# Kernel tuning notes

Measured on AMD Instinct MI355X. Metric: run time of the kernel, lower is better.

The kernel has to match this reference:

```python
import jax, jax.numpy as jnp
import numpy as np

N = 100000      # nodes
E = 1600000     # edges
F_IN = 64       # num_features
H = 64          # nhid
G = 512         # num graphs in batch
C = 2           # num_classes
BN_EPS = 1e-5


def setup_inputs() -> dict:
    key = jax.random.key(0)
    ks = jax.random.split(key, 8)
    x = jax.random.normal(ks[0], (N, F_IN), jnp.float32)
    edge_index = jax.random.randint(ks[1], (2, E), 0, N, dtype=jnp.int64)
    batch = jnp.sort(jax.random.randint(ks[2], (N,), 0, G, dtype=jnp.int64))
    s = lambda k, shp, fan: (jax.random.normal(k, shp, jnp.float32) / np.sqrt(fan)).astype(jnp.float32)
    W1 = s(ks[3], (F_IN, H), F_IN); b1 = jnp.zeros((H,), jnp.float32)
    W2 = s(ks[4], (H, H), H);       b2 = jnp.zeros((H,), jnp.float32)
    Wg = s(ks[5], (H, 1), H);       bg = jnp.zeros((1,), jnp.float32)
    bn_gamma = jnp.ones((H,), jnp.float32); bn_beta = jnp.zeros((H,), jnp.float32)
    bn_mean = jnp.zeros((H,), jnp.float32); bn_var = jnp.ones((H,), jnp.float32)
    W_lin = s(ks[6], (H, C), H);    b_lin = jnp.zeros((C,), jnp.float32)
    return dict(x=x, edge_index=edge_index, batch=batch,
                W1=W1, b1=b1, W2=W2, b2=b2, Wg=Wg, bg=bg,
                bn_gamma=bn_gamma, bn_beta=bn_beta, bn_mean=bn_mean, bn_var=bn_var,
                W_lin=W_lin, b_lin=b_lin)


def reference(x, edge_index, batch, W1, b1, W2, b2, Wg, bg,
              bn_gamma, bn_beta, bn_mean, bn_var, W_lin, b_lin):
    src, dst = edge_index[0], edge_index[1]
    # GINConv (eps=0): h_i = MLP(x_i + sum_{j->i} x_j)
    agg = jax.ops.segment_sum(x[src], dst, num_segments=N)       # [N, F_IN]
    h = x + agg
    h = jnp.maximum(h @ W1 + b1, 0.0) @ W2 + b2                  # [N, H]
    h = jnp.maximum(h, 0.0)                                      # outer ReLU
    # Attentional aggregation: segment softmax of gate, weighted segment-sum
    gate = (h @ Wg + bg)[:, 0]                                   # [N]
    gmax = jax.ops.segment_max(gate, batch, num_segments=G)      # [G]
    ex = jnp.exp(gate - gmax[batch])                             # [N]
    denom = jax.ops.segment_sum(ex, batch, num_segments=G)       # [G]
    alpha = ex / denom[batch]                                    # [N]
    pooled = jax.ops.segment_sum(alpha[:, None] * h, batch, num_segments=G)  # [G, H]
    # BatchNorm1d in eval mode (running stats); dropout is identity in eval
    norm = (pooled - bn_mean) / jnp.sqrt(bn_var + BN_EPS) * bn_gamma + bn_beta
    logits = norm @ W_lin + b_lin                                # [G, C]
    return jax.nn.log_softmax(logits, axis=-1)
```

## Files before the change

kernel.cpp:

```cpp
#include <hip/hip_runtime.h>
#include <math.h>
#include <float.h>

#define BN_EPS 1e-5f
#define PBLK   8192
#define NBUCKP 832
#define ACAP   4096
#define STCAP  2048

typedef short s16x8 __attribute__((ext_vector_type(8)));
typedef float f32x4 __attribute__((ext_vector_type(4)));

__device__ __forceinline__ unsigned short f2bf(float f) {
    unsigned u = __float_as_uint(f);
    u += 0x7FFFu + ((u >> 16) & 1u);
    return (unsigned short)(u >> 16);
}
__device__ __forceinline__ float bf2f(unsigned short b) {
    return __uint_as_float(((unsigned)b) << 16);
}

__global__ __launch_bounds__(512) void prep_partition(
    const float* __restrict__ x, unsigned short* __restrict__ xb,
    const float* __restrict__ W1, const float* __restrict__ W2,
    unsigned short* __restrict__ w1t, unsigned short* __restrict__ w2t,
    const int* __restrict__ src, const int* __restrict__ dst,
    const int* __restrict__ batch, int* __restrict__ gstart,
    int* __restrict__ bcur0, int* __restrict__ packed2,
    int N, int E, int EB, int G)
{
    __shared__ int hist[NBUCKP], lstart[NBUCKP], goff[NBUCKP], cur[NBUCKP];
    __shared__ int sorted[PBLK];
    __shared__ unsigned short sbkt[PBLK];

    int tid = threadIdx.x;
    int lane = tid & 63;
    int blk = blockIdx.x;

    int n4 = N * 16;
    for (int i = blk * 512 + tid; i < n4; i += gridDim.x * 512) {
        float4 f = *(const float4*)(x + (size_t)i * 4);
        ushort4 o;
        o.x = f2bf(f.x); o.y = f2bf(f.y); o.z = f2bf(f.z); o.w = f2bf(f.w);
        *(ushort4*)(xb + (size_t)i * 4) = o;
    }
    for (int i = blk * 512 + tid; i < N; i += gridDim.x * 512) {
        int bi = batch[i];
        int bp = (i == 0) ? -1 : batch[i - 1];
        for (int g = bp + 1; g <= bi; ++g) gstart[g] = i;
        if (i == N - 1)
            for (int g = bi + 1; g <= G; ++g) gstart[g] = N;
    }
    if (blk == 0)
        for (int idx = tid; idx < 4096; idx += 512)
            w1t[idx] = f2bf(W1[(idx & 63) * 64 + (idx >> 6)]);
    if (blk == 1)
        for (int idx = tid; idx < 4096; idx += 512)
            w2t[idx] = f2bf(W2[(idx & 63) * 64 + (idx >> 6)]);

    if (blk >= EB) return;

    int e0 = blk * PBLK;
    int cnt = E - e0; if (cnt > PBLK) cnt = PBLK; if (cnt < 0) cnt = 0;

    for (int i = tid; i < NBUCKP; i += 512) hist[i] = 0;
    __syncthreads();
    for (int i = tid; i < cnt; i += 512)
        atomicAdd(&hist[dst[e0 + i] >> 7], 1);
    __syncthreads();
    if (tid < 64) {
        int carry = 0;
        #pragma unroll
        for (int c = 0; c < NBUCKP / 64; ++c) {
            int idx = c * 64 + lane;
            int v = hist[idx];
            int xv = v;
            #pragma unroll
            for (int d = 1; d < 64; d <<= 1) {
                int t = __shfl_up(xv, d); if (lane >= d) xv += t;
            }
            lstart[idx] = xv - v + carry;
            carry += __shfl(xv, 63);
        }
    }
    __syncthreads();
    for (int i = tid; i < NBUCKP; i += 512) {
        cur[i] = lstart[i];
        if (hist[i] > 0) goff[i] = atomicAdd(&bcur0[i], hist[i]);
    }
    __syncthreads();
    for (int i = tid; i < cnt; i += 512) {
        int d = dst[e0 + i];
        int s = src[e0 + i];
        int b = d >> 7;
        int p = atomicAdd(&cur[b], 1);
        sorted[p] = ((d & 127) << 17) | s;
        sbkt[p] = (unsigned short)b;
    }
    __syncthreads();
    for (int i = tid; i < cnt; i += 512) {
        int b = sbkt[i];
        packed2[(size_t)b * ACAP + goff[b] + (i - lstart[b])] = sorted[i];
    }
}

__global__ __launch_bounds__(256) void bucket_fused(
    const unsigned short* __restrict__ xb,
    const int* __restrict__ packed2, const int* __restrict__ bcur0,
    const unsigned short* __restrict__ w1t, const unsigned short* __restrict__ w2t,
    const float* __restrict__ b1, const float* __restrict__ b2,
    const float* __restrict__ Wg, const float* __restrict__ bg,
    unsigned short* __restrict__ h_out, float* __restrict__ gate_out, int N)
{
    __shared__ int hist[64], excl[65], cur[64];
    __shared__ int stage[STCAP];
    __shared__ unsigned short vt[64][72];

    int tid = threadIdx.x;
    int lane = tid & 63;
    int wave = tid >> 6;
    int bh = blockIdx.x;
    int bk = bh >> 1;
    int half = bh & 1;
    int node0 = bh * 64;
    int ecnt = bcur0[bk];
    if (ecnt > ACAP) ecnt = ACAP;
    const int* arena = packed2 + (size_t)bk * ACAP;

    if (tid < 64) hist[tid] = 0;
    __syncthreads();
    for (int i = tid; i < ecnt; i += 256) {
        int v = arena[i];
        if ((v >> 23) == half)
            atomicAdd(&hist[(v >> 17) & 63], 1);
    }
    __syncthreads();
    if (tid < 64) {
        int v = hist[lane];
        int xv = v;
        #pragma unroll
        for (int d = 1; d < 64; d <<= 1) {
            int t = __shfl_up(xv, d); if (lane >= d) xv += t;
        }
        excl[lane] = xv - v;
        cur[lane]  = xv - v;
        if (lane == 63) excl[64] = xv;
    }
    __syncthreads();
    for (int i = tid; i < ecnt; i += 256) {
        int v = arena[i];
        if ((v >> 23) == half) {
            int p = atomicAdd(&cur[(v >> 17) & 63], 1);
            if (p < STCAP) stage[p] = v & 0x1FFFF;
        }
    }
    __syncthreads();

    int rowbase = wave * 16;
    for (int m = 0; m < 16; ++m) {
        int ln = rowbase + m;
        int node = node0 + ln;
        if (node < N) {
            int beg = excl[ln];     if (beg > STCAP) beg = STCAP;
            int end = excl[ln + 1]; if (end > STCAP) end = STCAP;

            float v0 = bf2f(xb[(size_t)node * 64 + lane]);
            float v1 = 0.f, v2 = 0.f, v3 = 0.f, v4 = 0.f, v5 = 0.f, v6 = 0.f, v7 = 0.f;

            for (int base = beg; base < end; base += 64) {
                int ei = (base + lane < end) ? stage[base + lane] : 0;
                int cnt = end - base; if (cnt > 64) cnt = 64;
                int j = 0;
                for (; j + 8 <= cnt; j += 8) {
                    int s0 = __builtin_amdgcn_readlane(ei, j + 0);
                    int s1 = __builtin_amdgcn_readlane(ei, j + 1);
                    int s2 = __builtin_amdgcn_readlane(ei, j + 2);
                    int s3 = __builtin_amdgcn_readlane(ei, j + 3);
                    int s4 = __builtin_amdgcn_readlane(ei, j + 4);
                    int s5 = __builtin_amdgcn_readlane(ei, j + 5);
                    int s6 = __builtin_amdgcn_readlane(ei, j + 6);
                    int s7 = __builtin_amdgcn_readlane(ei, j + 7);
                    unsigned short t0 = xb[(size_t)s0 * 64 + lane];
                    unsigned short t1 = xb[(size_t)s1 * 64 + lane];
                    unsigned short t2 = xb[(size_t)s2 * 64 + lane];
                    unsigned short t3 = xb[(size_t)s3 * 64 + lane];
                    unsigned short t4 = xb[(size_t)s4 * 64 + lane];
                    unsigned short t5 = xb[(size_t)s5 * 64 + lane];
                    unsigned short t6 = xb[(size_t)s6 * 64 + lane];
                    unsigned short t7 = xb[(size_t)s7 * 64 + lane];
                    v0 += bf2f(t0); v1 += bf2f(t1); v2 += bf2f(t2); v3 += bf2f(t3);
                    v4 += bf2f(t4); v5 += bf2f(t5); v6 += bf2f(t6); v7 += bf2f(t7);
                }
                for (; j + 4 <= cnt; j += 4) {
                    int s0 = __builtin_amdgcn_readlane(ei, j + 0);
                    int s1 = __builtin_amdgcn_readlane(ei, j + 1);
                    int s2 = __builtin_amdgcn_readlane(ei, j + 2);
                    int s3 = __builtin_amdgcn_readlane(ei, j + 3);
                    unsigned short t0 = xb[(size_t)s0 * 64 + lane];
                    unsigned short t1 = xb[(size_t)s1 * 64 + lane];
                    unsigned short t2 = xb[(size_t)s2 * 64 + lane];
                    unsigned short t3 = xb[(size_t)s3 * 64 + lane];
                    v4 += bf2f(t0); v5 += bf2f(t1); v6 += bf2f(t2); v7 += bf2f(t3);
                }
                for (; j < cnt; ++j) {
                    int s = __builtin_amdgcn_readlane(ei, j);
                    v1 += bf2f(xb[(size_t)s * 64 + lane]);
                }
            }
            float v = ((v0 + v1) + (v2 + v3)) + ((v4 + v5) + (v6 + v7));
            vt[ln][lane] = f2bf(v);
        } else {
            vt[ln][lane] = 0;
        }
    }

    {
        int quad = lane >> 4;
        int col  = lane & 15;

        s16x8 a0 = *(const s16x8*)&vt[rowbase + col][quad * 8];
        s16x8 a1 = *(const s16x8*)&vt[rowbase + col][32 + quad * 8];

        float b1v[4], b2v[4], wgv[4];
        #pragma unroll
        for (int nt = 0; nt < 4; ++nt) {
            b1v[nt] = b1[nt * 16 + col];
            b2v[nt] = b2[nt * 16 + col];
            wgv[nt] = Wg[nt * 16 + col];
        }
        float bgv = bg[0];

        f32x4 acc1[4];
        #pragma unroll
        for (int nt = 0; nt < 4; ++nt) {
            int off = (nt * 16 + col) * 64 + quad * 8;
            s16x8 w0 = *(const s16x8*)(w1t + off);
            s16x8 w1 = *(const s16x8*)(w1t + off + 32);
            f32x4 c = {0.f, 0.f, 0.f, 0.f};
            c = __builtin_amdgcn_mfma_f32_16x16x32_bf16(a0, w0, c, 0, 0, 0);
            c = __builtin_amdgcn_mfma_f32_16x16x32_bf16(a1, w1, c, 0, 0, 0);
            acc1[nt] = c;
        }
        #pragma unroll
        for (int nt = 0; nt < 4; ++nt)
            #pragma unroll
            for (int r = 0; r < 4; ++r) {
                float hv = fmaxf(acc1[nt][r] + b1v[nt], 0.f);
                vt[rowbase + quad * 4 + r][nt * 16 + col] = f2bf(hv);
            }

        s16x8 g0 = *(const s16x8*)&vt[rowbase + col][quad * 8];
        s16x8 g1 = *(const s16x8*)&vt[rowbase + col][32 + quad * 8];

        f32x4 acc2[4];
        #pragma unroll
        for (int nt = 0; nt < 4; ++nt) {
            int off = (nt * 16 + col) * 64 + quad * 8;
            s16x8 w0 = *(const s16x8*)(w2t + off);
            s16x8 w1 = *(const s16x8*)(w2t + off + 32);
            f32x4 c = {0.f, 0.f, 0.f, 0.f};
            c = __builtin_amdgcn_mfma_f32_16x16x32_bf16(g0, w0, c, 0, 0, 0);
            c = __builtin_amdgcn_mfma_f32_16x16x32_bf16(g1, w1, c, 0, 0, 0);
            acc2[nt] = c;
        }

        int nbase = node0 + rowbase;
        float gp[4] = {0.f, 0.f, 0.f, 0.f};
        #pragma unroll
        for (int nt = 0; nt < 4; ++nt)
            #pragma unroll
            for (int r = 0; r < 4; ++r) {
                float hv = fmaxf(acc2[nt][r] + b2v[nt], 0.f);
                int node = nbase + quad * 4 + r;
                if (node < N)
                    h_out[(size_t)node * 64 + nt * 16 + col] = f2bf(hv);
                gp[r] = fmaf(hv, wgv[nt], gp[r]);
            }
        #pragma unroll
        for (int r = 0; r < 4; ++r) {
            float t = gp[r];
            t += __shfl_xor(t, 1);
            t += __shfl_xor(t, 2);
            t += __shfl_xor(t, 4);
            t += __shfl_xor(t, 8);
            int node = nbase + quad * 4 + r;
            if (col == 0 && node < N) gate_out[node] = t + bgv;
        }
    }
}

__global__ __launch_bounds__(256) void pool_final(
    const unsigned short* __restrict__ h, const float* __restrict__ gate,
    const int* __restrict__ gstart,
    const float* __restrict__ gamma_, const float* __restrict__ beta_,
    const float* __restrict__ mean_, const float* __restrict__ var_,
    const float* __restrict__ Wl, const float* __restrict__ bl,
    float* __restrict__ out)
{
    int g = blockIdx.x;
    int tid = threadIdx.x;

    int start = gstart[g];
    int end   = gstart[g + 1];

    __shared__ float red[4];
    __shared__ float pool_s[4 * 64];

    int lane = tid & 63;
    int wave = tid >> 6;

    float m = -FLT_MAX;
    for (int i = start + tid; i < end; i += 256) m = fmaxf(m, gate[i]);
    #pragma unroll
    for (int off = 32; off; off >>= 1) m = fmaxf(m, __shfl_xor(m, off));
    if (lane == 0) red[wave] = m;
    __syncthreads();
    m = fmaxf(fmaxf(red[0], red[1]), fmaxf(red[2], red[3]));
    __syncthreads();

    float s = 0.f;
    for (int i = start + tid; i < end; i += 256) s += expf(gate[i] - m);
    #pragma unroll
    for (int off = 32; off; off >>= 1) s += __shfl_xor(s, off);
    if (lane == 0) red[wave] = s;
    __syncthreads();
    s = red[0] + red[1] + red[2] + red[3];

    float a0 = 0.f, a1 = 0.f, a2 = 0.f, a3 = 0.f;
    int i = start + wave;
    for (; i + 12 < end; i += 16) {
        float e0 = expf(gate[i]      - m);
        float e1 = expf(gate[i + 4]  - m);
        float e2 = expf(gate[i + 8]  - m);
        float e3 = expf(gate[i + 12] - m);
        float t0 = bf2f(h[(size_t)(i)      * 64 + lane]);
        float t1 = bf2f(h[(size_t)(i + 4)  * 64 + lane]);
        float t2 = bf2f(h[(size_t)(i + 8)  * 64 + lane]);
        float t3 = bf2f(h[(size_t)(i + 12) * 64 + lane]);
        a0 = fmaf(e0, t0, a0);
        a1 = fmaf(e1, t1, a1);
        a2 = fmaf(e2, t2, a2);
        a3 = fmaf(e3, t3, a3);
    }
    for (; i < end; i += 4) {
        float e = expf(gate[i] - m);
        a0 = fmaf(e, bf2f(h[(size_t)i * 64 + lane]), a0);
    }
    pool_s[wave * 64 + lane] = (a0 + a1) + (a2 + a3);
    __syncthreads();

    if (wave == 0) {
        float p = pool_s[lane] + pool_s[64 + lane] + pool_s[128 + lane] + pool_s[192 + lane];
        p = (end > start) ? (p / s) : 0.f;
        float nrm = (p - mean_[lane]) / sqrtf(var_[lane] + BN_EPS) * gamma_[lane] + beta_[lane];
        float l0 = nrm * Wl[lane * 2 + 0];
        float l1 = nrm * Wl[lane * 2 + 1];
        #pragma unroll
        for (int off = 32; off; off >>= 1) {
            l0 += __shfl_xor(l0, off);
            l1 += __shfl_xor(l1, off);
        }
        if (lane == 0) {
            l0 += bl[0];
            l1 += bl[1];
            float mx = fmaxf(l0, l1);
            float lse = mx + logf(expf(l0 - mx) + expf(l1 - mx));
            out[g * 2 + 0] = l0 - lse;
            out[g * 2 + 1] = l1 - lse;
        }
    }
}

extern "C" void kernel_launch(void* const* d_in, const int* in_sizes, int n_in,
                              void* d_out, int out_size, void* d_ws, size_t ws_size,
                              hipStream_t stream)
{
    const float* x     = (const float*)d_in[0];
    const int*   eidx  = (const int*)d_in[1];
    const int*   batch = (const int*)d_in[2];
    const float* W1    = (const float*)d_in[3];
    const float* b1    = (const float*)d_in[4];
    const float* W2    = (const float*)d_in[5];
    const float* b2    = (const float*)d_in[6];
    const float* Wg    = (const float*)d_in[7];
    const float* bg    = (const float*)d_in[8];
    const float* bng   = (const float*)d_in[9];
    const float* bnb   = (const float*)d_in[10];
    const float* bnm   = (const float*)d_in[11];
    const float* bnv   = (const float*)d_in[12];
    const float* Wl    = (const float*)d_in[13];
    const float* bl    = (const float*)d_in[14];
    float* out = (float*)d_out;

    int N = in_sizes[0] / 64;
    int E = in_sizes[1] / 2;
    int G = out_size / 2;
    int NP = ((N + 63) / 64) * 64;
    int NBUCK = (N + 127) / 128;
    int NHALF = (N + 63) / 64;
    int EB = (E + PBLK - 1) / PBLK;
    int GRID_A = 1024 > EB ? 1024 : EB;

    char* w = (char*)d_ws;
    int* packed2 = (int*)w;                     w += (size_t)NBUCK * ACAP * 4;
    unsigned short* hxb  = (unsigned short*)w;  w += (size_t)NP * 64 * 2;
    float* gate  = (float*)w;                   w += ((size_t)N * 4 + 255) / 256 * 256;
    int* bcur0   = (int*)w;                     w += NBUCKP * 4;
    unsigned short* w1t = (unsigned short*)w;   w += 4096 * 2;
    unsigned short* w2t = (unsigned short*)w;   w += 4096 * 2;
    int* gstart  = (int*)w;                     w += ((size_t)(G + 1) * 4 + 255) / 256 * 256;
    unsigned short* hbuf = (unsigned short*)w;

    const int* src = eidx;
    const int* dst = eidx + E;

    hipMemsetAsync(bcur0, 0, NBUCKP * sizeof(int), stream);

    prep_partition<<<GRID_A, 512, 0, stream>>>(x, hxb, W1, W2, w1t, w2t,
                                               src, dst, batch, gstart,
                                               bcur0, packed2,
                                               N, E, EB, G);

    bucket_fused  <<<NHALF, 256, 0, stream>>>(hxb, packed2, bcur0, w1t, w2t,
                                              b1, b2, Wg, bg, hbuf, gate, N);

    pool_final    <<<G, 256, 0, stream>>>(hbuf, gate, gstart, bng, bnb, bnm, bnv,
                                          Wl, bl, out);
}
```

Before: 216.0 us.

## Sort buckets in place per 128-node block and drop LDS staging

The partition kernel now uses smaller per-block chunks and scatters edges straight to the global bucket arenas, with no LDS sort-then-copy pass. The fused kernel now handles a whole 128-node bucket with 512 threads. It reads the arena once into registers, counting-sorts it back in place in global memory, and prefetches each node's next edge list while the current one is processed. The MFMA operand tile moves to an XOR-swizzled LDS layout to avoid bank conflicts. In exchange, the in-place global sort relies on the arena being private to each block, the scatter stores in the partition kernel are uncoalesced, and the 8-register edge capture assumes each bucket holds at most 4096 edges.

Measured after the change: 205.3 us. 1.05x faster.

```diff
diff --git a/kernel.cpp b/kernel.cpp
--- a/kernel.cpp
+++ b/kernel.cpp
@@ -3,10 +3,9 @@
 #include <float.h>
 
 #define BN_EPS 1e-5f
-#define PBLK   8192
+#define PBLK   2048
 #define NBUCKP 832
 #define ACAP   4096
-#define STCAP  2048
 
 typedef short s16x8 __attribute__((ext_vector_type(8)));
 typedef float f32x4 __attribute__((ext_vector_type(4)));
@@ -18,6 +17,9 @@
 }
 __device__ __forceinline__ float bf2f(unsigned short b) {
     return __uint_as_float(((unsigned)b) << 16);
+}
+__device__ __forceinline__ int vtb(int row, int byteoff) {
+    return row * 128 + (byteoff ^ ((row & 7) << 4));
 }
 
 __global__ __launch_bounds__(512) void prep_partition(
@@ -30,8 +32,6 @@
     int N, int E, int EB, int G)
 {
     __shared__ int hist[NBUCKP], lstart[NBUCKP], goff[NBUCKP], cur[NBUCKP];
-    __shared__ int sorted[PBLK];
-    __shared__ unsigned short sbkt[PBLK];
 
     int tid = threadIdx.x;
     int lane = tid & 63;
@@ -80,137 +80,159 @@
                 int t = __shfl_up(xv, d); if (lane >= d) xv += t;
             }
             lstart[idx] = xv - v + carry;
+            cur[idx]    = xv - v + carry;
             carry += __shfl(xv, 63);
         }
     }
     __syncthreads();
-    for (int i = tid; i < NBUCKP; i += 512) {
-        cur[i] = lstart[i];
+    for (int i = tid; i < NBUCKP; i += 512)
         if (hist[i] > 0) goff[i] = atomicAdd(&bcur0[i], hist[i]);
-    }
     __syncthreads();
     for (int i = tid; i < cnt; i += 512) {
         int d = dst[e0 + i];
         int s = src[e0 + i];
         int b = d >> 7;
         int p = atomicAdd(&cur[b], 1);
-        sorted[p] = ((d & 127) << 17) | s;
-        sbkt[p] = (unsigned short)b;
-    }
-    __syncthreads();
-    for (int i = tid; i < cnt; i += 512) {
-        int b = sbkt[i];
-        packed2[(size_t)b * ACAP + goff[b] + (i - lstart[b])] = sorted[i];
-    }
-}
-
-__global__ __launch_bounds__(256) void bucket_fused(
+        packed2[(size_t)b * ACAP + goff[b] + (p - lstart[b])] = ((d & 127) << 17) | s;
+    }
+}
+
+__global__ __launch_bounds__(512) void bucket_fused(
     const unsigned short* __restrict__ xb,
-    const int* __restrict__ packed2, const int* __restrict__ bcur0,
+    int* __restrict__ packed2, const int* __restrict__ bcur0,
     const unsigned short* __restrict__ w1t, const unsigned short* __restrict__ w2t,
     const float* __restrict__ b1, const float* __restrict__ b2,
     const float* __restrict__ Wg, const float* __restrict__ bg,
     unsigned short* __restrict__ h_out, float* __restrict__ gate_out, int N)
 {
-    __shared__ int hist[64], excl[65], cur[64];
-    __shared__ int stage[STCAP];
-    __shared__ unsigned short vt[64][72];
+    __shared__ char vt_raw[16384];
+    int* hist = (int*)vt_raw;
+    int* cur  = hist + 128;
+    int* excl = (int*)(vt_raw + 1024);
 
     int tid = threadIdx.x;
     int lane = tid & 63;
     int wave = tid >> 6;
-    int bh = blockIdx.x;
-    int bk = bh >> 1;
-    int half = bh & 1;
-    int node0 = bh * 64;
-    int ecnt = bcur0[bk];
+    int b = blockIdx.x;
+    int node0 = b * 128;
+    int ecnt = bcur0[b];
     if (ecnt > ACAP) ecnt = ACAP;
-    const int* arena = packed2 + (size_t)bk * ACAP;
-
-    if (tid < 64) hist[tid] = 0;
-    __syncthreads();
-    for (int i = tid; i < ecnt; i += 256) {
-        int v = arena[i];
-        if ((v >> 23) == half)
-            atomicAdd(&hist[(v >> 17) & 63], 1);
-    }
-    __syncthreads();
+    int* arena = packed2 + (size_t)b * ACAP;
+
+    if (tid < 128) hist[tid] = 0;
+    __syncthreads();
+
+    int ev[8];
+    #pragma unroll
+    for (int k = 0; k < 8; ++k) {
+        int i = tid + k * 512;
+        int val = -1;
+        if (i < ecnt) {
+            val = arena[i];
+            atomicAdd(&hist[val >> 17], 1);
+        }
+        ev[k] = val;
+    }
+    __syncthreads();
+
     if (tid < 64) {
-        int v = hist[lane];
-        int xv = v;
-        #pragma unroll
-        for (int d = 1; d < 64; d <<= 1) {
-            int t = __shfl_up(xv, d); if (lane >= d) xv += t;
-        }
-        excl[lane] = xv - v;
-        cur[lane]  = xv - v;
-        if (lane == 63) excl[64] = xv;
-    }
-    __syncthreads();
-    for (int i = tid; i < ecnt; i += 256) {
-        int v = arena[i];
-        if ((v >> 23) == half) {
-            int p = atomicAdd(&cur[(v >> 17) & 63], 1);
-            if (p < STCAP) stage[p] = v & 0x1FFFF;
+        int carry = 0;
+        #pragma unroll
+        for (int c = 0; c < 2; ++c) {
+            int idx = c * 64 + lane;
+            int v = hist[idx];
+            int xv = v;
+            #pragma unroll
+            for (int d = 1; d < 64; d <<= 1) {
+                int t = __shfl_up(xv, d); if (lane >= d) xv += t;
+            }
+            excl[idx] = xv - v + carry;
+            cur[idx]  = xv - v + carry;
+            carry += __shfl(xv, 63);
+        }
+        if (lane == 0) excl[128] = carry;
+    }
+    __syncthreads();
+
+    #pragma unroll
+    for (int k = 0; k < 8; ++k) {
+        int val = ev[k];
+        if (val >= 0) {
+            int p = atomicAdd(&cur[val >> 17], 1);
+            arena[p] = val & 0x1FFFF;
         }
     }
     __syncthreads();
 
     int rowbase = wave * 16;
-    for (int m = 0; m < 16; ++m) {
-        int ln = rowbase + m;
-        int node = node0 + ln;
-        if (node < N) {
-            int beg = excl[ln];     if (beg > STCAP) beg = STCAP;
-            int end = excl[ln + 1]; if (end > STCAP) end = STCAP;
-
-            float v0 = bf2f(xb[(size_t)node * 64 + lane]);
-            float v1 = 0.f, v2 = 0.f, v3 = 0.f, v4 = 0.f, v5 = 0.f, v6 = 0.f, v7 = 0.f;
-
-            for (int base = beg; base < end; base += 64) {
-                int ei = (base + lane < end) ? stage[base + lane] : 0;
-                int cnt = end - base; if (cnt > 64) cnt = 64;
-                int j = 0;
-                for (; j + 8 <= cnt; j += 8) {
-                    int s0 = __builtin_amdgcn_readlane(ei, j + 0);
-                    int s1 = __builtin_amdgcn_readlane(ei, j + 1);
-                    int s2 = __builtin_amdgcn_readlane(ei, j + 2);
-                    int s3 = __builtin_amdgcn_readlane(ei, j + 3);
-                    int s4 = __builtin_amdgcn_readlane(ei, j + 4);
-                    int s5 = __builtin_amdgcn_readlane(ei, j + 5);
-                    int s6 = __builtin_amdgcn_readlane(ei, j + 6);
-                    int s7 = __builtin_amdgcn_readlane(ei, j + 7);
-                    unsigned short t0 = xb[(size_t)s0 * 64 + lane];
-                    unsigned short t1 = xb[(size_t)s1 * 64 + lane];
-                    unsigned short t2 = xb[(size_t)s2 * 64 + lane];
-                    unsigned short t3 = xb[(size_t)s3 * 64 + lane];
-                    unsigned short t4 = xb[(size_t)s4 * 64 + lane];
-                    unsigned short t5 = xb[(size_t)s5 * 64 + lane];
-                    unsigned short t6 = xb[(size_t)s6 * 64 + lane];
-                    unsigned short t7 = xb[(size_t)s7 * 64 + lane];
-                    v0 += bf2f(t0); v1 += bf2f(t1); v2 += bf2f(t2); v3 += bf2f(t3);
-                    v4 += bf2f(t4); v5 += bf2f(t5); v6 += bf2f(t6); v7 += bf2f(t7);
+    int exv = excl[rowbase + (lane < 17 ? lane : 16)];
+    __syncthreads();
+
+    {
+        int beg  = __builtin_amdgcn_readlane(exv, 0);
+        int end_ = __builtin_amdgcn_readlane(exv, 1);
+        int ei   = (beg + lane < end_) ? arena[beg + lane] : 0;
+
+        for (int m = 0; m < 16; ++m) {
+            int cbeg = beg, cend = end_, cei = ei;
+            if (m < 15) {
+                beg  = end_;
+                end_ = __builtin_amdgcn_readlane(exv, m + 2);
+                ei   = (beg + lane < end_) ? arena[beg + lane] : 0;
+            }
+            int ln = rowbase + m;
+            int node = node0 + ln;
+            if (node < N) {
+                float v0 = bf2f(xb[(size_t)node * 64 + lane]);
+                float v1 = 0.f, v2 = 0.f, v3 = 0.f, v4 = 0.f, v5 = 0.f, v6 = 0.f, v7 = 0.f;
+
+                int eiv = cei;
+                for (int base = cbeg; base < cend; base += 64) {
+                    if (base != cbeg)
+                        eiv = (base + lane < cend) ? arena[base + lane] : 0;
+                    int cnt = cend - base; if (cnt > 64) cnt = 64;
+                    int j = 0;
+                    for (; j + 8 <= cnt; j += 8) {
+                        int s0 = __builtin_amdgcn_readlane(eiv, j + 0);
+                        int s1 = __builtin_amdgcn_readlane(eiv, j + 1);
+                        int s2 = __builtin_amdgcn_readlane(eiv, j + 2);
+                        int s3 = __builtin_amdgcn_readlane(eiv, j + 3);
+                        int s4 = __builtin_amdgcn_readlane(eiv, j + 4);
+                        int s5 = __builtin_amdgcn_readlane(eiv, j + 5);
+                        int s6 = __builtin_amdgcn_readlane(eiv, j + 6);
+                        int s7 = __builtin_amdgcn_readlane(eiv, j + 7);
+                        unsigned short t0 = xb[(size_t)s0 * 64 + lane];
+                        unsigned short t1 = xb[(size_t)s1 * 64 + lane];
+                        unsigned short t2 = xb[(size_t)s2 * 64 + lane];
+                        unsigned short t3 = xb[(size_t)s3 * 64 + lane];
+                        unsigned short t4 = xb[(size_t)s4 * 64 + lane];
+                        unsigned short t5 = xb[(size_t)s5 * 64 + lane];
+                        unsigned short t6 = xb[(size_t)s6 * 64 + lane];
+                        unsigned short t7 = xb[(size_t)s7 * 64 + lane];
+                        v0 += bf2f(t0); v1 += bf2f(t1); v2 += bf2f(t2); v3 += bf2f(t3);
+                        v4 += bf2f(t4); v5 += bf2f(t5); v6 += bf2f(t6); v7 += bf2f(t7);
+                    }
+                    for (; j + 4 <= cnt; j += 4) {
+                        int s0 = __builtin_amdgcn_readlane(eiv, j + 0);
+                        int s1 = __builtin_amdgcn_readlane(eiv, j + 1);
+                        int s2 = __builtin_amdgcn_readlane(eiv, j + 2);
+                        int s3 = __builtin_amdgcn_readlane(eiv, j + 3);
+                        unsigned short t0 = xb[(size_t)s0 * 64 + lane];
+                        unsigned short t1 = xb[(size_t)s1 * 64 + lane];
+                        unsigned short t2 = xb[(size_t)s2 * 64 + lane];
+                        unsigned short t3 = xb[(size_t)s3 * 64 + lane];
+                        v4 += bf2f(t0); v5 += bf2f(t1); v6 += bf2f(t2); v7 += bf2f(t3);
+                    }
+                    for (; j < cnt; ++j) {
+                        int s = __builtin_amdgcn_readlane(eiv, j);
+                        v1 += bf2f(xb[(size_t)s * 64 + lane]);
+                    }
                 }
-                for (; j + 4 <= cnt; j += 4) {
-                    int s0 = __builtin_amdgcn_readlane(ei, j + 0);
-                    int s1 = __builtin_amdgcn_readlane(ei, j + 1);
-                    int s2 = __builtin_amdgcn_readlane(ei, j + 2);
-                    int s3 = __builtin_amdgcn_readlane(ei, j + 3);
-                    unsigned short t0 = xb[(size_t)s0 * 64 + lane];
-                    unsigned short t1 = xb[(size_t)s1 * 64 + lane];
-                    unsigned short t2 = xb[(size_t)s2 * 64 + lane];
-                    unsigned short t3 = xb[(size_t)s3 * 64 + lane];
-                    v4 += bf2f(t0); v5 += bf2f(t1); v6 += bf2f(t2); v7 += bf2f(t3);
-                }
-                for (; j < cnt; ++j) {
-                    int s = __builtin_amdgcn_readlane(ei, j);
-                    v1 += bf2f(xb[(size_t)s * 64 + lane]);
-                }
-            }
-            float v = ((v0 + v1) + (v2 + v3)) + ((v4 + v5) + (v6 + v7));
-            vt[ln][lane] = f2bf(v);
-        } else {
-            vt[ln][lane] = 0;
+                float v = ((v0 + v1) + (v2 + v3)) + ((v4 + v5) + (v6 + v7));
+                *(unsigned short*)(vt_raw + vtb(ln, lane * 2)) = f2bf(v);
+            } else {
+                *(unsigned short*)(vt_raw + vtb(ln, lane * 2)) = 0;
+            }
         }
     }
 
@@ -218,8 +240,8 @@
         int quad = lane >> 4;
         int col  = lane & 15;
 
-        s16x8 a0 = *(const s16x8*)&vt[rowbase + col][quad * 8];
-        s16x8 a1 = *(const s16x8*)&vt[rowbase + col][32 + quad * 8];
+        s16x8 a0 = *(const s16x8*)(vt_raw + vtb(rowbase + col, quad * 16));
+        s16x8 a1 = *(const s16x8*)(vt_raw + vtb(rowbase + col, 64 + quad * 16));
 
         float b1v[4], b2v[4], wgv[4];
         #pragma unroll
@@ -246,11 +268,11 @@
             #pragma unroll
             for (int r = 0; r < 4; ++r) {
                 float hv = fmaxf(acc1[nt][r] + b1v[nt], 0.f);
-                vt[rowbase + quad * 4 + r][nt * 16 + col] = f2bf(hv);
-            }
-
-        s16x8 g0 = *(const s16x8*)&vt[rowbase + col][quad * 8];
-        s16x8 g1 = *(const s16x8*)&vt[rowbase + col][32 + quad * 8];
+                *(unsigned short*)(vt_raw + vtb(rowbase + quad * 4 + r, (nt * 16 + col) * 2)) = f2bf(hv);
+            }
+
+        s16x8 g0 = *(const s16x8*)(vt_raw + vtb(rowbase + col, quad * 16));
+        s16x8 g1 = *(const s16x8*)(vt_raw + vtb(rowbase + col, 64 + quad * 16));
 
         f32x4 acc2[4];
         #pragma unroll
@@ -397,7 +419,6 @@
     int G = out_size / 2;
     int NP = ((N + 63) / 64) * 64;
     int NBUCK = (N + 127) / 128;
-    int NHALF = (N + 63) / 64;
     int EB = (E + PBLK - 1) / PBLK;
     int GRID_A = 1024 > EB ? 1024 : EB;
 
@@ -421,7 +442,7 @@
                                                bcur0, packed2,
                                                N, E, EB, G);
 
-    bucket_fused  <<<NHALF, 256, 0, stream>>>(hxb, packed2, bcur0, w1t, w2t,
+    bucket_fused  <<<NBUCK, 512, 0, stream>>>(hxb, packed2, bcur0, w1t, w2t,
                                               b1, b2, Wg, bg, hbuf, gate, N);
 
     pool_final    <<<G, 256, 0, stream>>>(hbuf, gate, gstart, bng, bnb, bnm, bnv,
```
